# Performance work log

Measured on AMD Instinct MI355X. Metric: run time of the kernel, lower is better.

The kernel has to match this reference:

```python
import jax, jax.numpy as jnp
import numpy as np

S, B, D, H, F = 2048, 4, 1024, 2, 2048
HD = D // H  # head dim = 512
EPS = 1e-8   # forward() hardcodes 1e-8, ignoring init eps


def rmsnorm(x, w):
    ms = jnp.mean(x * x, axis=-1, keepdims=True)
    return w * (x / jnp.sqrt(ms + EPS))


def setup_inputs() -> dict:
    key = jax.random.key(0)
    ks = jax.random.split(key, 12)
    s = 0.02
    return {
        "x": jax.random.normal(ks[0], (S, B, D), jnp.float32),
        "w_norm1": 1.0 + s * jax.random.normal(ks[1], (D,), jnp.float32),
        "in_proj_w": s * jax.random.normal(ks[2], (3 * D, D), jnp.float32),
        "in_proj_b": s * jax.random.normal(ks[3], (3 * D,), jnp.float32),
        "out_proj_w": s * jax.random.normal(ks[4], (D, D), jnp.float32),
        "out_proj_b": s * jax.random.normal(ks[5], (D,), jnp.float32),
        "w_norm2": 1.0 + s * jax.random.normal(ks[6], (D,), jnp.float32),
        "W1": s * jax.random.normal(ks[7], (F, D), jnp.float32),
        "b1": s * jax.random.normal(ks[8], (F,), jnp.float32),
        "W2": s * jax.random.normal(ks[9], (D, F), jnp.float32),
        "b2": s * jax.random.normal(ks[10], (D,), jnp.float32),
    }


def reference(x, w_norm1, in_proj_w, in_proj_b, out_proj_w, out_proj_b,
              w_norm2, W1, b1, W2, b2):
    # pre-norm
    h = rmsnorm(x, w_norm1)                      # (S,B,D)
    # packed qkv projection (torch MultiheadAttention in_proj)
    qkv = h @ in_proj_w.T + in_proj_b            # (S,B,3D)
    q, k, v = jnp.split(qkv, 3, axis=-1)
    # (S,B,D) -> (B,H,S,HD)
    def heads(t):
        return t.reshape(S, B, H, HD).transpose(1, 2, 0, 3)
    q, k, v = heads(q), heads(k), heads(v)
    scores = jnp.einsum("bhsd,bhtd->bhst", q, k) / jnp.sqrt(jnp.float32(HD))
    causal = jnp.tril(jnp.ones((S, S), bool))
    scores = jnp.where(causal, scores, -jnp.inf)
    attn = jax.nn.softmax(scores, axis=-1)       # (B,H,S,S)
    ctx = jnp.einsum("bhst,bhtd->bhsd", attn, v)  # (B,H,S,HD)
    ctx = ctx.transpose(2, 0, 1, 3).reshape(S, B, D)
    attn_out = ctx @ out_proj_w.T + out_proj_b
    # residual 1
    x1 = x + attn_out
    # MLP: Linear -> exact GELU -> Linear
    m = rmsnorm(x1, w_norm2)
    mlp = jax.nn.gelu(m @ W1.T + b1, approximate=False) @ W2.T + b2
    return x1 + mlp
```

## Files before the change

kernel.cpp:

```cpp
#include <hip/hip_runtime.h>


typedef __bf16 bf16;
typedef bf16 bf16x8 __attribute__((ext_vector_type(8)));
typedef bf16 bf16x4 __attribute__((ext_vector_type(4)));
typedef float f32x4 __attribute__((ext_vector_type(4)));

#define MFMA16x16x32(A, B, C) __builtin_amdgcn_mfma_f32_16x16x32_bf16(A, B, C, 0, 0, 0)

__device__ __forceinline__ void gload16(const void* g, void* l) {
  __builtin_amdgcn_global_load_lds(
      (const __attribute__((address_space(1))) void*)g,
      (__attribute__((address_space(3))) void*)l, 16, 0, 0);
}

__global__ __launch_bounds__(256) void wcvt4(
    const float* __restrict__ s0, bf16* __restrict__ d0,
    const float* __restrict__ s1, bf16* __restrict__ d1,
    const float* __restrict__ s2, bf16* __restrict__ d2,
    const float* __restrict__ s3, bf16* __restrict__ d3)
{
  const int gid = blockIdx.x * 256 + threadIdx.x;
  const float* s; bf16* d; int off;
  if (gid < 786432)       { s = s0; d = d0; off = gid; }
  else if (gid < 1048576) { s = s1; d = d1; off = gid - 786432; }
  else if (gid < 1572864) { s = s2; d = d2; off = gid - 1048576; }
  else                    { s = s3; d = d3; off = gid - 1572864; }
  const int i = off * 4;
  const float4 v = *(const float4*)(s + i);
  bf16x4 o;
  o[0] = (bf16)v.x; o[1] = (bf16)v.y; o[2] = (bf16)v.z; o[3] = (bf16)v.w;
  *(bf16x4*)(d + i) = o;
}

__global__ __launch_bounds__(256) void rmsnorm_kernel(
    const float* __restrict__ x, const float* __restrict__ w, bf16* __restrict__ out)
{
  const int row = blockIdx.x;
  const int tid = threadIdx.x;
  const float4 v = *(const float4*)(x + (size_t)row * 1024 + tid * 4);
  float ss = v.x * v.x + v.y * v.y + v.z * v.z + v.w * v.w;
#pragma unroll
  for (int off = 1; off < 64; off <<= 1) ss += __shfl_xor(ss, off, 64);
  __shared__ float red[4];
  if ((tid & 63) == 0) red[tid >> 6] = ss;
  __syncthreads();
  const float tot = red[0] + red[1] + red[2] + red[3];
  const float inv = rsqrtf(tot * (1.0f / 1024.0f) + 1e-8f);
  const float4 g = *(const float4*)(w + tid * 4);
  bf16x4 o;
  o[0] = (bf16)(v.x * g.x * inv);
  o[1] = (bf16)(v.y * g.y * inv);
  o[2] = (bf16)(v.z * g.z * inv);
  o[3] = (bf16)(v.w * g.w * inv);
  *(bf16x4*)(out + (size_t)row * 1024 + tid * 4) = o;
}

enum { EPI_BF16 = 0, EPI_RES = 1, EPI_GELU = 2, EPI_QKV = 3 };

template <int EPI>
__global__ __launch_bounds__(256, 4) void gemm_bt2(
    const bf16* __restrict__ A,
    const bf16* __restrict__ B,
    const float* __restrict__ bias,
    const float* res,
    float* outF, bf16* outQ, bf16* outK, bf16* outV,
    int M, int N, int K)
{
  __shared__ bf16 lds[2][8192];
  const int tid = threadIdx.x;
  const int Nb = N >> 7;
  const int lin = blockIdx.x;
  const int sup = lin / (Nb << 4);
  const int rem = lin - sup * (Nb << 4);
  const int bm = (sup << 4) + (rem & 15);
  const int bn = rem >> 4;
  const int w = tid >> 6, lane = tid & 63;
  const int q = lane >> 4, lr = lane & 15;
  const int wr = (w >> 1) * 64, wc = (w & 1) * 64;
  f32x4 acc[4][4] = {};
  const int srow = lane >> 2;
  const int gch = ((lane & 3) - ((lane >> 3) & 3)) & 3;
  const bf16* Ab = A + (size_t)(bm * 128) * K;
  const bf16* Bb = B + (size_t)(bn * 128) * K;
  const int sw = ((q + (lr >> 1)) & 3) * 16;
  const int NK = K >> 5;

#define STAGE(dst, k0)                                                        \
  {                                                                           \
    bf16* De = (dst);                                                         \
    _Pragma("unroll")                                                         \
    for (int c = 0; c < 2; c++) {                                             \
      const int r = (w * 2 + c) * 16 + srow;                                  \
      gload16(Ab + (size_t)r * K + (k0) + gch * 8, De + (w * 2 + c) * 512);   \
      gload16(Bb + (size_t)r * K + (k0) + gch * 8, De + 4096 + (w * 2 + c) * 512); \
    }                                                                         \
  }

  STAGE(&lds[0][0], 0);
  __syncthreads();
#pragma unroll 1
  for (int u = 0; u < NK; ++u) {
    bf16* cur = &lds[u & 1][0];
    bf16* nxt = &lds[(u + 1) & 1][0];
    if (u + 1 < NK) STAGE(nxt, (u + 1) * 32);
    const char* As = (const char*)cur;
    const char* Bs = (const char*)(cur + 4096);
    bf16x8 af[4], bfr[4];
#pragma unroll
    for (int mt = 0; mt < 4; mt++)
      af[mt] = *(const bf16x8*)(As + (wr + mt * 16 + lr) * 64 + sw);
#pragma unroll
    for (int nt = 0; nt < 4; nt++)
      bfr[nt] = *(const bf16x8*)(Bs + (wc + nt * 16 + lr) * 64 + sw);
#pragma unroll
    for (int mt = 0; mt < 4; mt++)
#pragma unroll
      for (int nt = 0; nt < 4; nt++)
        acc[mt][nt] = MFMA16x16x32(af[mt], bfr[nt], acc[mt][nt]);
    __syncthreads();
  }
#undef STAGE

  const int gm0 = bm * 128 + wr + q * 4;
  const int gn0 = bn * 128 + wc + lr;
  bf16* outs = nullptr;
  if constexpr (EPI == EPI_QKV) {
    const int reg = (bn * 128) >> 10;
    outs = reg == 0 ? outQ : (reg == 1 ? outK : outV);
  } else {
    outs = outQ;
  }
#pragma unroll
  for (int nt = 0; nt < 4; nt++) {
    const int gn = gn0 + nt * 16;
    const float bv = bias[gn];
#pragma unroll
    for (int mt = 0; mt < 4; mt++) {
#pragma unroll
      for (int r = 0; r < 4; r++) {
        float v = acc[mt][nt][r] + bv;
        const int gm = gm0 + mt * 16 + r;
        if constexpr (EPI == EPI_GELU) {
          v = 0.5f * v * (1.0f + erff(v * 0.70710678118654752f));
          outs[(size_t)gm * N + gn] = (bf16)v;
        } else if constexpr (EPI == EPI_BF16) {
          outs[(size_t)gm * N + gn] = (bf16)v;
        } else if constexpr (EPI == EPI_QKV) {
          outs[(size_t)gm * 1024 + (gn & 1023)] = (bf16)v;
        } else {
          const size_t idx = (size_t)gm * N + gn;
          outF[idx] = v + res[idx];
        }
      }
    }
  }
}

__global__ __launch_bounds__(256) void vtrans_kernel(
    const bf16* __restrict__ vtmp, bf16* __restrict__ vt)
{
  __shared__ bf16 tile[64 * 72];
  const int kt = blockIdx.x;
  const int dt = blockIdx.y;
  const int bh = blockIdx.z;
  const int b = bh >> 1, h = bh & 1;
  const int tid = threadIdx.x;
#pragma unroll
  for (int it = 0; it < 2; it++) {
    const int key = it * 32 + (tid >> 3);
    const int dc = (tid & 7) * 8;
    const bf16x8 v = *(const bf16x8*)(vtmp +
        (size_t)((kt * 64 + key) * 4 + b) * 1024 + h * 512 + dt * 64 + dc);
    *(bf16x8*)&tile[key * 72 + dc] = v;
  }
  __syncthreads();
#pragma unroll
  for (int it = 0; it < 2; it++) {
    const int dim = it * 32 + (tid >> 3);
    const int kc = (tid & 7) * 8;
    bf16x8 o;
#pragma unroll
    for (int j = 0; j < 8; j++) o[j] = tile[(kc + j) * 72 + dim];
    *(bf16x8*)(vt + (size_t)bh * (1u << 20) +
               (size_t)(dt * 64 + dim) * 2048 + kt * 64 + kc) = o;
  }
}

__global__ __launch_bounds__(768, 3) void attn_kernel(
    const bf16* __restrict__ qb, const bf16* __restrict__ kb,
    const bf16* __restrict__ vtg, bf16* __restrict__ opart,
    float* __restrict__ lpart)
{
  __shared__ bf16 Ks[2][64 * 520];
  __shared__ bf16 Ps[2][4][16 * 72];
  const int bh = blockIdx.x;
  const int y = blockIdx.y;
  const int b = bh >> 1, h = bh & 1;
  const int tid = threadIdx.x;
  const int w = tid >> 6, lane = tid & 63;
  const int q = lane >> 4, lr = lane & 15;
  const float sc = 0.044194173824159216f;

  if (w < 4) {
    const bf16* krow0 = kb + (size_t)b * 1024 + h * 512 + lane * 8;
    for (int piece = 0; piece < 2; ++piece) {
      const int qt = piece ? (31 - y) : y;
      const int qrow0 = qt * 64;
      const int nc = qt + 1;
      const int hs = (nc + 1) >> 1;
      const int c0 = piece ? hs : 0;
      const int c1 = piece ? nc : hs;
      bf16x8 Qf[16];
      {
        const bf16* qp = qb + (size_t)((qrow0 + w * 16 + lr) * 4 + b) * 1024 + h * 512 + q * 8;
#pragma unroll
        for (int kk = 0; kk < 16; kk++) Qf[kk] = *(const bf16x8*)(qp + kk * 32);
      }
#pragma unroll
      for (int j = 0; j < 16; j++)
        gload16(krow0 + (size_t)((c0 * 64 + w * 16 + j) * 4) * 1024,
                &Ks[c0 & 1][(w * 16 + j) * 520]);
      __syncthreads();
      const int myrow = qrow0 + w * 16 + q * 4;
      for (int t = c0; t <= c1; t++) {
        if (t < c1) {
          const int p = t & 1;
          const int kc = t * 64;
          if (t + 1 < c1) {
            const int kc2 = (t + 1) * 64;
#pragma unroll
            for (int j = 0; j < 16; j++)
              gload16(krow0 + (size_t)((kc2 + w * 16 + j) * 4) * 1024,
                      &Ks[1 - p][(w * 16 + j) * 520]);
          }
          f32x4 S0 = {}, S1 = {}, S2 = {}, S3 = {};
#pragma unroll
          for (int kk = 0; kk < 16; kk++) {
            const bf16x8 k0 = *(const bf16x8*)&Ks[p][lr * 520 + kk * 32 + q * 8];
            const bf16x8 k1 = *(const bf16x8*)&Ks[p][(16 + lr) * 520 + kk * 32 + q * 8];
            const bf16x8 k2 = *(const bf16x8*)&Ks[p][(32 + lr) * 520 + kk * 32 + q * 8];
            const bf16x8 k3 = *(const bf16x8*)&Ks[p][(48 + lr) * 520 + kk * 32 + q * 8];
            S0 = MFMA16x16x32(Qf[kk], k0, S0);
            S1 = MFMA16x16x32(Qf[kk], k1, S1);
            S2 = MFMA16x16x32(Qf[kk], k2, S2);
            S3 = MFMA16x16x32(Qf[kk], k3, S3);
          }
#pragma unroll
          for (int r = 0; r < 4; r++) {
            const int row = myrow + r;
            const float p0 = (kc + lr > row) ? 0.f : __expf(S0[r] * sc);
            const float p1 = (kc + 16 + lr > row) ? 0.f : __expf(S1[r] * sc);
            const float p2 = (kc + 32 + lr > row) ? 0.f : __expf(S2[r] * sc);
            const float p3 = (kc + 48 + lr > row) ? 0.f : __expf(S3[r] * sc);
            bf16* pr = &Ps[p][w][(q * 4 + r) * 72];
            pr[lr] = (bf16)p0;
            pr[16 + lr] = (bf16)p1;
            pr[32 + lr] = (bf16)p2;
            pr[48 + lr] = (bf16)p3;
          }
        }
        __syncthreads();
      }
    }
  } else {
    const int pw = w - 4;
    bf16x8 ones;
#pragma unroll
    for (int e = 0; e < 8; e++) ones[e] = (bf16)1.0f;
    const bf16* vbase = vtg + ((size_t)bh << 20) + (size_t)(pw * 64 + lr) * 2048 + q * 8;
    for (int piece = 0; piece < 2; ++piece) {
      const int qt = piece ? (31 - y) : y;
      const int qrow0 = qt * 64;
      const int nc = qt + 1;
      const int hs = (nc + 1) >> 1;
      const int c0 = piece ? hs : 0;
      const int c1 = piece ? nc : hs;
      f32x4 O[4][4] = {};
      f32x4 lac = {};
      __syncthreads();
      for (int t = c0; t <= c1; t++) {
        if (t > c0) {
          const int p = (t - 1) & 1;
          const int kc = (t - 1) * 64;
#pragma unroll
          for (int s = 0; s < 2; s++) {
            bf16x8 pa[4];
#pragma unroll
            for (int rt = 0; rt < 4; rt++)
              pa[rt] = *(const bf16x8*)&Ps[p][rt][lr * 72 + s * 32 + q * 8];
            if (pw < 4) {
              const bf16x8 psel = pw == 0 ? pa[0] : (pw == 1 ? pa[1] : (pw == 2 ? pa[2] : pa[3]));
              lac = MFMA16x16x32(psel, ones, lac);
            }
#pragma unroll
            for (int ct = 0; ct < 4; ct++) {
              const bf16x8 vf = *(const bf16x8*)(vbase + (size_t)(ct * 16) * 2048 + kc + s * 32);
#pragma unroll
              for (int rt = 0; rt < 4; rt++)
                O[rt][ct] = MFMA16x16x32(pa[rt], vf, O[rt][ct]);
            }
          }
        }
        __syncthreads();
      }
      bf16* op = opart + (size_t)piece * (8u << 20) + (size_t)bh * (1u << 20);
#pragma unroll
      for (int rt = 0; rt < 4; rt++)
#pragma unroll
        for (int ct = 0; ct < 4; ct++)
#pragma unroll
          for (int r = 0; r < 4; r++)
            op[(size_t)(qrow0 + rt * 16 + q * 4 + r) * 512 + pw * 64 + ct * 16 + lr] =
                (bf16)O[rt][ct][r];
      if (lr == 0 && pw < 4) {
#pragma unroll
        for (int r = 0; r < 4; r++)
          lpart[piece * 16384 + bh * 2048 + qrow0 + pw * 16 + q * 4 + r] = lac[r];
      }
    }
  }
}

__global__ __launch_bounds__(256) void attn_combine(
    const bf16* __restrict__ opart, const float* __restrict__ lpart,
    bf16* __restrict__ ctx)
{
  const int gid = blockIdx.x * 256 + threadIdx.x;
  const int bh = gid >> 17;
  const int rem = gid & 131071;
  const int row = rem >> 6;
  const int dc = (rem & 63) * 8;
  const size_t o = (size_t)bh * (1u << 20) + (size_t)row * 512 + dc;
  const bf16x8 a = *(const bf16x8*)(opart + o);
  const bf16x8 c = *(const bf16x8*)(opart + (size_t)(8u << 20) + o);
  const float inv = 1.0f /
      (lpart[bh * 2048 + row] + lpart[16384 + bh * 2048 + row]);
  bf16x8 ov;
#pragma unroll
  for (int e = 0; e < 8; e++) ov[e] = (bf16)(((float)a[e] + (float)c[e]) * inv);
  const int b = bh >> 1, h = bh & 1;
  *(bf16x8*)(ctx + (size_t)(row * 4 + b) * 1024 + h * 512 + dc) = ov;
}

extern "C" void kernel_launch(void* const* d_in, const int* in_sizes, int n_in,
                              void* d_out, int out_size, void* d_ws, size_t ws_size,
                              hipStream_t stream)
{
  (void)in_sizes; (void)n_in; (void)out_size; (void)ws_size;
  const float* x    = (const float*)d_in[0];
  const float* wn1  = (const float*)d_in[1];
  const float* wqkv = (const float*)d_in[2];
  const float* bqkv = (const float*)d_in[3];
  const float* wout = (const float*)d_in[4];
  const float* bout = (const float*)d_in[5];
  const float* wn2  = (const float*)d_in[6];
  const float* W1   = (const float*)d_in[7];
  const float* b1   = (const float*)d_in[8];
  const float* W2   = (const float*)d_in[9];
  const float* b2   = (const float*)d_in[10];
  float* out = (float*)d_out;

  char* ws = (char*)d_ws;
  const size_t Mi = 1u << 20;
  bf16* S0v = (bf16*)(ws);
  bf16* S1v = (bf16*)(ws + 16 * Mi);
  bf16* S2v = (bf16*)(ws + 32 * Mi);
  bf16* S3v = (bf16*)(ws + 48 * Mi);
  bf16* wqb = (bf16*)(ws + 64 * Mi);
  bf16* wob = (bf16*)(ws + 70 * Mi);
  bf16* w1b = (bf16*)(ws + 72 * Mi);
  bf16* w2b = (bf16*)(ws + 76 * Mi);
  const int M = 8192;

  wcvt4<<<8192, 256, 0, stream>>>(wqkv, wqb, wout, wob, W1, w1b, W2, w2b);
  rmsnorm_kernel<<<8192, 256, 0, stream>>>(x, wn1, S0v);
  gemm_bt2<EPI_QKV><<<64 * 24, 256, 0, stream>>>(
      S0v, wqb, bqkv, nullptr, nullptr, S1v, S2v, S3v, M, 3072, 1024);
  vtrans_kernel<<<dim3(32, 8, 8), 256, 0, stream>>>(S3v, S0v);
  attn_kernel<<<dim3(8, 32), 768, 0, stream>>>(
      S1v, S2v, S0v, (bf16*)d_out, (float*)S3v);
  attn_combine<<<4096, 256, 0, stream>>>((const bf16*)d_out, (const float*)S3v, S1v);
  gemm_bt2<EPI_RES><<<64 * 8, 256, 0, stream>>>(
      S1v, wob, bout, x, out, nullptr, nullptr, nullptr, M, 1024, 1024);
  rmsnorm_kernel<<<8192, 256, 0, stream>>>(out, wn2, S0v);
  gemm_bt2<EPI_GELU><<<64 * 16, 256, 0, stream>>>(
      S0v, w1b, b1, nullptr, nullptr, S2v, nullptr, nullptr, M, 2048, 1024);
  gemm_bt2<EPI_RES><<<64 * 8, 256, 0, stream>>>(
      S2v, w2b, b2, out, out, nullptr, nullptr, nullptr, M, 1024, 2048);
}
```

Measured before the change: 418.1 us.

## Use 256x256-tile pipelined GEMM with XCD-aware block mapping for MLP up-projection

Adds a new 512-thread GEMM kernel with 256x256 output tiles, double-buffered LDS staged through direct global-to-LDS loads with an XOR swizzle, and staged loads interleaved between MFMA phases under s_setprio. Blocks are remapped so consecutive tiles land on the same XCD. It replaces the generic gemm_bt2 for the W1+GELU projection. The goal is more data reuse and better overlap of loads with compute. In exchange it uses 128KB of LDS per block and launches only 256 blocks, which risks low occupancy and tail imbalance.

```diff
diff --git a/kernel.cpp b/kernel.cpp
--- a/kernel.cpp
+++ b/kernel.cpp
@@ -157,6 +157,149 @@
   }
 }
 
+__global__ __launch_bounds__(512, 2) void gemm256p(
+    const bf16* __restrict__ A,
+    const bf16* __restrict__ B,
+    const float* __restrict__ bias,
+    bf16* __restrict__ outO,
+    int M, int N, int K)
+{
+  __shared__ __align__(16) char ldsb[131072];
+  const int tid = threadIdx.x;
+  const int w = tid >> 6, lane = tid & 63;
+  const int q = lane >> 4, lr = lane & 15;
+  const int wm = w >> 2, wn = w & 3;
+  const int nbn = N >> 8;
+  const int cpx = gridDim.x >> 3;
+  const int lin = blockIdx.x;
+  const int wg = (lin & 7) * cpx + (lin >> 3);
+  const int bm = wg / nbn, bn = wg - bm * nbn;
+  const bf16* Ab = A + (size_t)(bm * 256) * K;
+  const bf16* Bb = B + (size_t)(bn * 256) * K;
+  f32x4 acc[8][4] = {};
+  const int NK = K >> 6;
+
+  const int rA = tid >> 3;
+  const int stgc = (((tid & 7) * 16) ^ (((tid >> 3) & 3) << 5)) >> 1;
+  const int x5 = (lr & 3) << 5;
+  const int in0 = (q * 16) ^ x5;
+  const int in1 = (64 + q * 16) ^ x5;
+  const char* bmyc0;
+
+#define STG(bufoff, sect, srcp)                                               \
+  {                                                                           \
+    gload16((srcp) + (size_t)rA * K, ldsb + (bufoff) + (sect) + tid * 16);    \
+    gload16((srcp) + (size_t)(rA + 64) * K,                                   \
+            ldsb + (bufoff) + (sect) + 8192 + tid * 16);                      \
+  }
+
+  STG(0, 0,     Ab + stgc);
+  STG(0, 16384, Ab + (size_t)128 * K + stgc);
+  STG(0, 32768, Bb + stgc);
+  STG(0, 49152, Bb + (size_t)128 * K + stgc);
+
+  bf16x8 af[4][2], bfv[4][2];
+#pragma unroll 1
+  for (int u = 0; u < NK; ++u) {
+    const int cu = (u & 1) << 16;
+    const int nb = ((u + 1) & 1) << 16;
+    const int kn = (u + 1) << 6;
+    const bool st = (u + 1 < NK);
+    const char* amy = ldsb + cu + wm * 16384;
+    const char* bmy = ldsb + cu + 32768 + (wn >> 1) * 16384;
+    const int brow = (wn & 1) * 64;
+    if (st) { STG(nb, 0, Ab + kn + stgc); }
+    if (st) asm volatile("s_waitcnt vmcnt(2)");
+    else    asm volatile("s_waitcnt vmcnt(0)");
+    asm volatile("s_barrier" ::: "memory");
+#pragma unroll
+    for (int m2 = 0; m2 < 4; m2++) {
+      af[m2][0] = *(const bf16x8*)(amy + (m2 * 16 + lr) * 128 + in0);
+      af[m2][1] = *(const bf16x8*)(amy + (m2 * 16 + lr) * 128 + in1);
+    }
+#pragma unroll
+    for (int n2 = 0; n2 < 2; n2++) {
+      bfv[n2][0] = *(const bf16x8*)(bmy + (brow + n2 * 16 + lr) * 128 + in0);
+      bfv[n2][1] = *(const bf16x8*)(bmy + (brow + n2 * 16 + lr) * 128 + in1);
+    }
+    __builtin_amdgcn_s_setprio(1);
+#pragma unroll
+    for (int m2 = 0; m2 < 4; m2++)
+#pragma unroll
+      for (int n2 = 0; n2 < 2; n2++) {
+        acc[m2][n2] = MFMA16x16x32(af[m2][0], bfv[n2][0], acc[m2][n2]);
+        acc[m2][n2] = MFMA16x16x32(af[m2][1], bfv[n2][1], acc[m2][n2]);
+      }
+    __builtin_amdgcn_s_setprio(0);
+    __builtin_amdgcn_s_barrier();
+#pragma unroll
+    for (int n2 = 2; n2 < 4; n2++) {
+      bfv[n2][0] = *(const bf16x8*)(bmy + (brow + n2 * 16 + lr) * 128 + in0);
+      bfv[n2][1] = *(const bf16x8*)(bmy + (brow + n2 * 16 + lr) * 128 + in1);
+    }
+    if (st) { STG(nb, 16384, Ab + (size_t)128 * K + kn + stgc); }
+    __builtin_amdgcn_s_barrier();
+    __builtin_amdgcn_s_setprio(1);
+#pragma unroll
+    for (int m2 = 0; m2 < 4; m2++)
+#pragma unroll
+      for (int n2 = 2; n2 < 4; n2++) {
+        acc[m2][n2] = MFMA16x16x32(af[m2][0], bfv[n2][0], acc[m2][n2]);
+        acc[m2][n2] = MFMA16x16x32(af[m2][1], bfv[n2][1], acc[m2][n2]);
+      }
+    __builtin_amdgcn_s_setprio(0);
+    __builtin_amdgcn_s_barrier();
+#pragma unroll
+    for (int m2 = 0; m2 < 4; m2++) {
+      af[m2][0] = *(const bf16x8*)(amy + ((m2 + 4) * 16 + lr) * 128 + in0);
+      af[m2][1] = *(const bf16x8*)(amy + ((m2 + 4) * 16 + lr) * 128 + in1);
+    }
+    if (st) { STG(nb, 32768, Bb + kn + stgc); }
+    __builtin_amdgcn_s_barrier();
+    __builtin_amdgcn_s_setprio(1);
+#pragma unroll
+    for (int m2 = 0; m2 < 4; m2++)
+#pragma unroll
+      for (int n2 = 0; n2 < 2; n2++) {
+        acc[m2 + 4][n2] = MFMA16x16x32(af[m2][0], bfv[n2][0], acc[m2 + 4][n2]);
+        acc[m2 + 4][n2] = MFMA16x16x32(af[m2][1], bfv[n2][1], acc[m2 + 4][n2]);
+      }
+    __builtin_amdgcn_s_setprio(0);
+    __builtin_amdgcn_s_barrier();
+    if (st) { STG(nb, 49152, Bb + (size_t)128 * K + kn + stgc); }
+    __builtin_amdgcn_s_barrier();
+    __builtin_amdgcn_s_setprio(1);
+#pragma unroll
+    for (int m2 = 0; m2 < 4; m2++)
+#pragma unroll
+      for (int n2 = 2; n2 < 4; n2++) {
+        acc[m2 + 4][n2] = MFMA16x16x32(af[m2][0], bfv[n2][0], acc[m2 + 4][n2]);
+        acc[m2 + 4][n2] = MFMA16x16x32(af[m2][1], bfv[n2][1], acc[m2 + 4][n2]);
+      }
+    __builtin_amdgcn_s_setprio(0);
+    __builtin_amdgcn_s_barrier();
+  }
+#undef STG
+  (void)bmyc0;
+
+  const int gm0 = bm * 256 + wm * 128 + q * 4;
+  const int gn0 = bn * 256 + wn * 64 + lr;
+#pragma unroll
+  for (int nt = 0; nt < 4; nt++) {
+    const int gn = gn0 + nt * 16;
+    const float bv = bias[gn];
+#pragma unroll
+    for (int mt = 0; mt < 8; mt++) {
+#pragma unroll
+      for (int r = 0; r < 4; r++) {
+        float v = acc[mt][nt][r] + bv;
+        v = 0.5f * v * (1.0f + erff(v * 0.70710678118654752f));
+        outO[(size_t)(gm0 + mt * 16 + r) * N + gn] = (bf16)v;
+      }
+    }
+  }
+}
+
 __global__ __launch_bounds__(256) void vtrans_kernel(
     const bf16* __restrict__ vtmp, bf16* __restrict__ vt)
 {
@@ -384,8 +527,7 @@
   gemm_bt2<EPI_RES><<<64 * 8, 256, 0, stream>>>(
       S1v, wob, bout, x, out, nullptr, nullptr, nullptr, M, 1024, 1024);
   rmsnorm_kernel<<<8192, 256, 0, stream>>>(out, wn2, S0v);
-  gemm_bt2<EPI_GELU><<<64 * 16, 256, 0, stream>>>(
-      S0v, w1b, b1, nullptr, nullptr, S2v, nullptr, nullptr, M, 2048, 1024);
+  gemm256p<<<256, 512, 0, stream>>>(S0v, w1b, b1, S2v, M, 2048, 1024);
   gemm_bt2<EPI_RES><<<64 * 8, 256, 0, stream>>>(
       S2v, w2b, b2, out, out, nullptr, nullptr, nullptr, M, 1024, 2048);
 }
```

Measured after the change: 427.6 us. 2.3% more time.
